# Optimization experiments

Measured on AMD Instinct MI355X. Metric: run time of the kernel, lower is better.

The kernel has to match this reference:

```python
import jax, jax.numpy as jnp
import numpy as np

B, S, E, H = 2, 2048, 1024, 16
HD = E // H  # head_dim = 64
NEG = jnp.float32(-1e9)


def setup_inputs() -> dict:
    key = jax.random.key(0)
    k1, k2, k3 = jax.random.split(key, 3)
    x = jax.random.normal(k1, (B, S, E), dtype=jnp.float32)
    w_qkv = jax.random.normal(k2, (E, 3 * E), dtype=jnp.float32) * 0.02
    b_qkv = jnp.zeros((3 * E,), dtype=jnp.float32)
    w_proj = jax.random.normal(k3, (E, E), dtype=jnp.float32) * 0.02
    b_proj = jnp.zeros((E,), dtype=jnp.float32)
    return {"x": x, "w_qkv": w_qkv, "b_qkv": b_qkv, "w_proj": w_proj, "b_proj": b_proj}


def reference(x, w_qkv, b_qkv, w_proj, b_proj):
    # c_attn (GPT2 Conv1D): x @ W + b -> [B,S,3E]
    qkv = x @ w_qkv + b_qkv
    q, k, v = jnp.split(qkv, 3, axis=-1)
    # split heads -> [B,H,S,HD]
    def heads(t):
        return t.reshape(B, S, H, HD).transpose(0, 2, 1, 3)
    q, k, v = heads(q), heads(k), heads(v)
    # scaled QK^T, causal mask, softmax (attn_pdrop=0 so dropout is identity)
    scores = jnp.einsum("bhqd,bhkd->bhqk", q, k) / jnp.sqrt(jnp.float32(HD))
    causal = jnp.tril(jnp.ones((S, S), dtype=bool))
    scores = jnp.where(causal, scores, NEG)
    attn = jax.nn.softmax(scores, axis=-1)
    out = jnp.einsum("bhqk,bhkd->bhqd", attn, v)
    out = out.transpose(0, 2, 1, 3).reshape(B, S, E)
    # c_proj
    return out @ w_proj + b_proj
```

## Files before the change

### kernel.cpp

```cpp
#include <hip/hip_runtime.h>


typedef __bf16 bf16;
typedef __bf16 bf16x4 __attribute__((ext_vector_type(4)));
typedef __bf16 bf16x8 __attribute__((ext_vector_type(8)));
typedef float f32x4 __attribute__((ext_vector_type(4)));

#define GLOBAL_AS(p) ((const __attribute__((address_space(1))) void*)(p))
#define LDS_AS(p) ((__attribute__((address_space(3))) void*)(p))

__device__ __forceinline__ void g2l16(const void* g, void* l) {
  __builtin_amdgcn_global_load_lds(GLOBAL_AS(g), LDS_AS(l), 16, 0, 0);
}

#define QSCL 0.18033688f

__global__ __launch_bounds__(256) void prep_kernel(
    const float* __restrict__ x, const float* __restrict__ wq,
    const float* __restrict__ wp, bf16* __restrict__ Xbf,
    bf16* __restrict__ Wqt, bf16* __restrict__ Wpt) {
  __shared__ float tile[32][33];
  const int t = threadIdx.x;
  const int b = blockIdx.x;
  if (b < 4096) {
    const int i = (b * 256 + t) * 4;
    const float4 v = *(const float4*)(x + i);
    bf16x4 o;
    o.x = (bf16)v.x; o.y = (bf16)v.y; o.z = (bf16)v.z; o.w = (bf16)v.w;
    *(bf16x4*)(Xbf + i) = o;
    return;
  }
  const float* W; bf16* Wt; int C, bx, by;
  if (b < 7168) {
    const int b2 = b - 4096;
    W = wq; Wt = Wqt; C = 3072; bx = b2 % 96; by = b2 / 96;
  } else {
    const int b3 = b - 7168;
    W = wp; Wt = Wpt; C = 1024; bx = b3 & 31; by = b3 >> 5;
  }
  const int c0 = bx * 32, r0 = by * 32;
  const int tx = t & 31, ty = t >> 5;
#pragma unroll
  for (int i = ty; i < 32; i += 8) tile[i][tx] = W[(r0 + i) * C + c0 + tx];
  __syncthreads();
#pragma unroll
  for (int i = ty; i < 32; i += 8)
    Wt[(c0 + i) * 1024 + r0 + tx] = (bf16)tile[tx][i];
}

template <int N, int EPI>
__global__ __launch_bounds__(256) void gemm_bt_kernel(
    const bf16* __restrict__ A, const bf16* __restrict__ Bt,
    const float* __restrict__ bias, float* __restrict__ Cf,
    bf16* __restrict__ Qo, bf16* __restrict__ Ko, bf16* __restrict__ Vo) {
  constexpr int K = 1024;
  __shared__ bf16 As[128 * 32];
  __shared__ bf16 Bs[128 * 32];
  const int t = threadIdx.x;
  const int m0 = blockIdx.x * 128;
  const int n0 = blockIdx.y * 128;
  const int wave = t >> 6, lane = t & 63;
  const int wr = (wave >> 1) * 64, wc = (wave & 1) * 64;
  const int lr = lane & 15, lg = lane >> 4;
  f32x4 acc[4][4] = {};
  const bf16* ag = A + (m0 + (t >> 2)) * K + (t & 3) * 8;
  const bf16* bg = Bt + (n0 + (t >> 2)) * K + (t & 3) * 8;
  for (int k0 = 0; k0 < K; k0 += 32) {
    __syncthreads();
    g2l16(ag, &As[t * 8]);
    g2l16(ag + 64 * K, &As[2048 + t * 8]);
    g2l16(bg, &Bs[t * 8]);
    g2l16(bg + 64 * K, &Bs[2048 + t * 8]);
    ag += 32; bg += 32;
    __syncthreads();
    bf16x8 af[4], bfr[4];
#pragma unroll
    for (int i = 0; i < 4; i++)
      af[i] = *(const bf16x8*)&As[(wr + i * 16 + lr) * 32 + lg * 8];
#pragma unroll
    for (int j = 0; j < 4; j++)
      bfr[j] = *(const bf16x8*)&Bs[(wc + j * 16 + lr) * 32 + lg * 8];
#pragma unroll
    for (int i = 0; i < 4; i++)
#pragma unroll
      for (int j = 0; j < 4; j++)
        acc[i][j] = __builtin_amdgcn_mfma_f32_16x16x32_bf16(af[i], bfr[j],
                                                            acc[i][j], 0, 0, 0);
  }
#pragma unroll
  for (int i = 0; i < 4; i++) {
#pragma unroll
    for (int j = 0; j < 4; j++) {
      const int n = n0 + wc + j * 16 + lr;
      const float bv = bias[n];
#pragma unroll
      for (int r = 0; r < 4; r++) {
        const int m = m0 + wr + i * 16 + lg * 4 + r;
        const float v = acc[i][j][r] + bv;
        if (EPI == 0) {
          Cf[m * N + n] = v;
        } else {
          const int b = m >> 11, s = m & 2047;
          const int reg = n >> 10, e = n & 1023;
          const int h = e >> 6, d = e & 63;
          bf16* dst = (reg == 0) ? Qo : (reg == 1) ? Ko : Vo;
          const float vv = (reg == 0) ? v * QSCL : v;
          dst[((b * 16 + h) * 2048 + s) * 64 + d] = (bf16)vv;
        }
      }
    }
  }
}

__global__ __launch_bounds__(256) void vtrans_kernel(
    const bf16* __restrict__ V, bf16* __restrict__ Vt) {
  __shared__ bf16 tile[64][72];
  const int t = threadIdx.x;
  const int bh = blockIdx.y;
  const int s0 = blockIdx.x * 64;
#pragma unroll
  for (int i = 0; i < 2; i++) {
    const int u = i * 256 + t;
    const int s = u >> 3, c = u & 7;
    *(bf16x8*)&tile[s][c * 8] =
        *(const bf16x8*)(V + ((size_t)bh * 2048 + s0 + s) * 64 + c * 8);
  }
  __syncthreads();
  {
    const int d = t >> 2, part = t & 3;
    bf16x8 o0, o1;
#pragma unroll
    for (int e = 0; e < 8; e++) {
      o0[e] = tile[part * 16 + e][d];
      o1[e] = tile[part * 16 + 8 + e][d];
    }
    bf16* dst = Vt + ((size_t)bh * 64 + d) * 2048 + s0 + part * 16;
    *(bf16x8*)dst = o0;
    *(bf16x8*)(dst + 8) = o1;
  }
}

__device__ __forceinline__ void stage_kv(const bf16* __restrict__ Kg,
                                         const bf16* __restrict__ Vg, int kb,
                                         bf16* ks, bf16* vs, int t) {
  int u = t, r = u >> 3, c = (u & 7) ^ (r & 7);
  g2l16(Kg + (kb + r) * 64 + c * 8, ks + u * 8);
  g2l16(Vg + r * 2048 + kb + c * 8, vs + u * 8);
  u = 256 + t; r = u >> 3; c = (u & 7) ^ (r & 7);
  g2l16(Kg + (kb + r) * 64 + c * 8, ks + u * 8);
  g2l16(Vg + r * 2048 + kb + c * 8, vs + u * 8);
}

__global__ __launch_bounds__(256, 3) void attn_kernel(
    const bf16* __restrict__ Qb, const bf16* __restrict__ Kb,
    const bf16* __restrict__ Vt, bf16* __restrict__ Obf) {
  __shared__ bf16 Ks[2][64 * 64];
  __shared__ bf16 Vs[2][64 * 64];
  __shared__ bf16 Ps[4][16 * 72];
  const int t = threadIdx.x;
  const int w = t >> 6, lane = t & 63;
  const int lr = lane & 15, lg = lane >> 4;
  const int bx = blockIdx.x;
  const int xcd = bx & 7, idx = bx >> 3;
  const int bh = (idx & 3) * 8 + xcd;
  const int strip = 31 - (idx >> 2);
  const int qb = strip * 64 + w * 16;
  const bf16* Qg = Qb + (size_t)bh * 2048 * 64;
  const bf16* Kg = Kb + (size_t)bh * 2048 * 64;
  const bf16* Vg = Vt + (size_t)bh * 64 * 2048;
  bf16x8 bq[2];
#pragma unroll
  for (int h = 0; h < 2; h++)
    bq[h] = *(const bf16x8*)(Qg + (qb + lr) * 64 + h * 32 + lg * 8);
  f32x4 oacc[4] = {};
  float lsum = 0.f;
  bf16* ps = &Ps[w][0];
  const int T = strip + 1;
  stage_kv(Kg, Vg, 0, Ks[0], Vs[0], t);
  for (int ti = 0; ti < T; ++ti) {
    __syncthreads();
    if (ti + 1 < T)
      stage_kv(Kg, Vg, (ti + 1) * 64, Ks[(ti + 1) & 1], Vs[(ti + 1) & 1], t);
    const int kb = ti * 64;
    const bf16* ks = Ks[ti & 1];
    const bf16* vs = Vs[ti & 1];
    bf16x8 ak[4][2], av[4][2];
#pragma unroll
    for (int j = 0; j < 4; j++) {
      const int row = j * 16 + lr;
#pragma unroll
      for (int h = 0; h < 2; h++)
        ak[j][h] =
            *(const bf16x8*)(ks + (row * 8 + ((h * 4 + lg) ^ (row & 7))) * 8);
    }
#pragma unroll
    for (int dt = 0; dt < 4; dt++) {
      const int row = dt * 16 + lr;
#pragma unroll
      for (int h = 0; h < 2; h++)
        av[dt][h] =
            *(const bf16x8*)(vs + (row * 8 + ((h * 4 + lg) ^ (row & 7))) * 8);
    }
    f32x4 sacc[4];
#pragma unroll
    for (int j = 0; j < 4; j++) {
      f32x4 s = {};
      s = __builtin_amdgcn_mfma_f32_16x16x32_bf16(ak[j][0], bq[0], s, 0, 0, 0);
      s = __builtin_amdgcn_mfma_f32_16x16x32_bf16(ak[j][1], bq[1], s, 0, 0, 0);
      sacc[j] = s;
    }
    const bool diag = (kb + 63 > qb);
    bf16x4 pk[4];
#pragma unroll
    for (int j = 0; j < 4; j++)
#pragma unroll
      for (int r = 0; r < 4; r++) {
        float v = sacc[j][r];
        if (diag && (kb + j * 16 + lg * 4 + r > qb + lr)) v = -1e30f;
        const float e = __builtin_amdgcn_exp2f(v);
        lsum += e;
        pk[j][r] = (bf16)e;
      }
    asm volatile("" ::: "memory");
#pragma unroll
    for (int j = 0; j < 4; j++)
      *(bf16x4*)(ps + lr * 72 + j * 16 + lg * 4) = pk[j];
    asm volatile("s_waitcnt lgkmcnt(0)" ::: "memory");
    bf16x8 bp[2];
#pragma unroll
    for (int h = 0; h < 2; h++)
      bp[h] = *(const bf16x8*)(ps + lr * 72 + h * 32 + lg * 8);
#pragma unroll
    for (int dt = 0; dt < 4; dt++) {
      f32x4 o = oacc[dt];
      o = __builtin_amdgcn_mfma_f32_16x16x32_bf16(av[dt][0], bp[0], o, 0, 0, 0);
      o = __builtin_amdgcn_mfma_f32_16x16x32_bf16(av[dt][1], bp[1], o, 0, 0, 0);
      oacc[dt] = o;
    }
  }
  lsum += __shfl_xor(lsum, 16, 64);
  lsum += __shfl_xor(lsum, 32, 64);
  const float inv = 1.0f / lsum;
  const int b = bh >> 4, hh = bh & 15;
  const int q = qb + lr;
  bf16* orow = Obf + ((size_t)(b * 2048 + q)) * 1024 + hh * 64;
#pragma unroll
  for (int dt = 0; dt < 4; dt++) {
    bf16x4 ov;
#pragma unroll
    for (int r = 0; r < 4; r++) ov[r] = (bf16)(oacc[dt][r] * inv);
    *(bf16x4*)(orow + dt * 16 + lg * 4) = ov;
  }
}

extern "C" void kernel_launch(void* const* d_in, const int* in_sizes, int n_in,
                              void* d_out, int out_size, void* d_ws,
                              size_t ws_size, hipStream_t stream) {
  const float* x      = (const float*)d_in[0];
  const float* w_qkv  = (const float*)d_in[1];
  const float* b_qkv  = (const float*)d_in[2];
  const float* w_proj = (const float*)d_in[3];
  const float* b_proj = (const float*)d_in[4];
  float* out = (float*)d_out;

  char* w = (char*)d_ws;
  bf16* Xbf = (bf16*)w;  w += 4096 * 1024 * 2;
  bf16* Wqt = (bf16*)w;  w += 3072 * 1024 * 2;
  bf16* Wpt = (bf16*)w;  w += 1024 * 1024 * 2;
  bf16* Qb  = (bf16*)w;  w += 2 * 16 * 2048 * 64 * 2;
  bf16* Kb  = (bf16*)w;  w += 2 * 16 * 2048 * 64 * 2;
  bf16* Vb  = (bf16*)w;  w += 2 * 16 * 2048 * 64 * 2;
  bf16* Obf = (bf16*)w;  w += 4096 * 1024 * 2;
  bf16* Vt  = Xbf;

  prep_kernel<<<8192, 256, 0, stream>>>(x, w_qkv, w_proj, Xbf, Wqt, Wpt);
  gemm_bt_kernel<3072, 1><<<dim3(32, 24), 256, 0, stream>>>(
      Xbf, Wqt, b_qkv, nullptr, Qb, Kb, Vb);
  vtrans_kernel<<<dim3(32, 32), 256, 0, stream>>>(Vb, Vt);
  attn_kernel<<<1024, 256, 0, stream>>>(Qb, Kb, Vt, Obf);
  gemm_bt_kernel<1024, 0><<<dim3(32, 8), 256, 0, stream>>>(
      Obf, Wpt, b_proj, out, nullptr, nullptr, nullptr);
}
```

Baseline: 181.5 us.

## Fuse V transpose into QKV GEMM, single-buffer attention, smaller proj tiles

The QKV GEMM epilogue now writes V directly in transposed [bh,d,s] layout with 4-wide stores, which removes the separate vtrans kernel and its extra round trip through memory. The attention kernel drops double-buffered K/V staging in favour of a single buffer with an extra barrier and raises its occupancy hint to 4 blocks per CU. This gives up load/compute overlap in exchange for more resident waves. The projection GEMM uses 64-row tiles so it launches twice as many blocks and fills more CUs.

```diff
diff --git a/kernel.cpp b/kernel.cpp
--- a/kernel.cpp
+++ b/kernel.cpp
@@ -48,11 +48,10 @@
     Wt[(c0 + i) * 1024 + r0 + tx] = (bf16)tile[tx][i];
 }
 
-template <int N, int EPI>
-__global__ __launch_bounds__(256) void gemm_bt_kernel(
+__global__ __launch_bounds__(256) void gemm_qkv_kernel(
     const bf16* __restrict__ A, const bf16* __restrict__ Bt,
-    const float* __restrict__ bias, float* __restrict__ Cf,
-    bf16* __restrict__ Qo, bf16* __restrict__ Ko, bf16* __restrict__ Vo) {
+    const float* __restrict__ bias, bf16* __restrict__ Qo,
+    bf16* __restrict__ Ko, bf16* __restrict__ Vto) {
   constexpr int K = 1024;
   __shared__ bf16 As[128 * 32];
   __shared__ bf16 Bs[128 * 32];
@@ -93,50 +92,78 @@
     for (int j = 0; j < 4; j++) {
       const int n = n0 + wc + j * 16 + lr;
       const float bv = bias[n];
+      if (n0 >= 2048) {
+        const int e = n & 1023, h = e >> 6, d = e & 63;
+        const int mb = m0 + wr + i * 16 + lg * 4;
+        const int b = mb >> 11, s = mb & 2047;
+        bf16x4 vv;
+#pragma unroll
+        for (int r = 0; r < 4; r++) vv[r] = (bf16)(acc[i][j][r] + bv);
+        *(bf16x4*)(Vto + ((size_t)((b * 16 + h) * 64 + d)) * 2048 + s) = vv;
+      } else {
+        const int e = n & 1023, h = e >> 6, d = e & 63;
+        const bool isq = (n < 1024);
+        bf16* dst = isq ? Qo : Ko;
+#pragma unroll
+        for (int r = 0; r < 4; r++) {
+          const int m = m0 + wr + i * 16 + lg * 4 + r;
+          const int b = m >> 11, s = m & 2047;
+          const float v = acc[i][j][r] + bv;
+          dst[((b * 16 + h) * 2048 + s) * 64 + d] = (bf16)(isq ? v * QSCL : v);
+        }
+      }
+    }
+  }
+}
+
+__global__ __launch_bounds__(256) void gemm_proj_kernel(
+    const bf16* __restrict__ A, const bf16* __restrict__ Bt,
+    const float* __restrict__ bias, float* __restrict__ Cf) {
+  constexpr int K = 1024, N = 1024;
+  __shared__ bf16 As[64 * 32];
+  __shared__ bf16 Bs[128 * 32];
+  const int t = threadIdx.x;
+  const int m0 = blockIdx.x * 64;
+  const int n0 = blockIdx.y * 128;
+  const int wave = t >> 6, lane = t & 63;
+  const int wr = (wave >> 1) * 32, wc = (wave & 1) * 64;
+  const int lr = lane & 15, lg = lane >> 4;
+  f32x4 acc[2][4] = {};
+  const bf16* ag = A + (m0 + (t >> 2)) * K + (t & 3) * 8;
+  const bf16* bg = Bt + (n0 + (t >> 2)) * K + (t & 3) * 8;
+  for (int k0 = 0; k0 < K; k0 += 32) {
+    __syncthreads();
+    g2l16(ag, &As[t * 8]);
+    g2l16(bg, &Bs[t * 8]);
+    g2l16(bg + 64 * K, &Bs[2048 + t * 8]);
+    ag += 32; bg += 32;
+    __syncthreads();
+    bf16x8 af[2], bfr[4];
+#pragma unroll
+    for (int i = 0; i < 2; i++)
+      af[i] = *(const bf16x8*)&As[(wr + i * 16 + lr) * 32 + lg * 8];
+#pragma unroll
+    for (int j = 0; j < 4; j++)
+      bfr[j] = *(const bf16x8*)&Bs[(wc + j * 16 + lr) * 32 + lg * 8];
+#pragma unroll
+    for (int i = 0; i < 2; i++)
+#pragma unroll
+      for (int j = 0; j < 4; j++)
+        acc[i][j] = __builtin_amdgcn_mfma_f32_16x16x32_bf16(af[i], bfr[j],
+                                                            acc[i][j], 0, 0, 0);
+  }
+#pragma unroll
+  for (int i = 0; i < 2; i++) {
+#pragma unroll
+    for (int j = 0; j < 4; j++) {
+      const int n = n0 + wc + j * 16 + lr;
+      const float bv = bias[n];
 #pragma unroll
       for (int r = 0; r < 4; r++) {
         const int m = m0 + wr + i * 16 + lg * 4 + r;
-        const float v = acc[i][j][r] + bv;
-        if (EPI == 0) {
-          Cf[m * N + n] = v;
-        } else {
-          const int b = m >> 11, s = m & 2047;
-          const int reg = n >> 10, e = n & 1023;
-          const int h = e >> 6, d = e & 63;
-          bf16* dst = (reg == 0) ? Qo : (reg == 1) ? Ko : Vo;
-          const float vv = (reg == 0) ? v * QSCL : v;
-          dst[((b * 16 + h) * 2048 + s) * 64 + d] = (bf16)vv;
-        }
+        Cf[m * N + n] = acc[i][j][r] + bv;
       }
     }
-  }
-}
-
-__global__ __launch_bounds__(256) void vtrans_kernel(
-    const bf16* __restrict__ V, bf16* __restrict__ Vt) {
-  __shared__ bf16 tile[64][72];
-  const int t = threadIdx.x;
-  const int bh = blockIdx.y;
-  const int s0 = blockIdx.x * 64;
-#pragma unroll
-  for (int i = 0; i < 2; i++) {
-    const int u = i * 256 + t;
-    const int s = u >> 3, c = u & 7;
-    *(bf16x8*)&tile[s][c * 8] =
-        *(const bf16x8*)(V + ((size_t)bh * 2048 + s0 + s) * 64 + c * 8);
-  }
-  __syncthreads();
-  {
-    const int d = t >> 2, part = t & 3;
-    bf16x8 o0, o1;
-#pragma unroll
-    for (int e = 0; e < 8; e++) {
-      o0[e] = tile[part * 16 + e][d];
-      o1[e] = tile[part * 16 + 8 + e][d];
-    }
-    bf16* dst = Vt + ((size_t)bh * 64 + d) * 2048 + s0 + part * 16;
-    *(bf16x8*)dst = o0;
-    *(bf16x8*)(dst + 8) = o1;
   }
 }
 
@@ -151,11 +178,11 @@
   g2l16(Vg + r * 2048 + kb + c * 8, vs + u * 8);
 }
 
-__global__ __launch_bounds__(256, 3) void attn_kernel(
+__global__ __launch_bounds__(256, 4) void attn_kernel(
     const bf16* __restrict__ Qb, const bf16* __restrict__ Kb,
     const bf16* __restrict__ Vt, bf16* __restrict__ Obf) {
-  __shared__ bf16 Ks[2][64 * 64];
-  __shared__ bf16 Vs[2][64 * 64];
+  __shared__ bf16 Ks[64 * 64];
+  __shared__ bf16 Vs[64 * 64];
   __shared__ bf16 Ps[4][16 * 72];
   const int t = threadIdx.x;
   const int w = t >> 6, lane = t & 63;
@@ -176,14 +203,11 @@
   float lsum = 0.f;
   bf16* ps = &Ps[w][0];
   const int T = strip + 1;
-  stage_kv(Kg, Vg, 0, Ks[0], Vs[0], t);
   for (int ti = 0; ti < T; ++ti) {
     __syncthreads();
-    if (ti + 1 < T)
-      stage_kv(Kg, Vg, (ti + 1) * 64, Ks[(ti + 1) & 1], Vs[(ti + 1) & 1], t);
+    stage_kv(Kg, Vg, ti * 64, Ks, Vs, t);
+    __syncthreads();
     const int kb = ti * 64;
-    const bf16* ks = Ks[ti & 1];
-    const bf16* vs = Vs[ti & 1];
     bf16x8 ak[4][2], av[4][2];
 #pragma unroll
     for (int j = 0; j < 4; j++) {
@@ -191,7 +215,7 @@
 #pragma unroll
       for (int h = 0; h < 2; h++)
         ak[j][h] =
-            *(const bf16x8*)(ks + (row * 8 + ((h * 4 + lg) ^ (row & 7))) * 8);
+            *(const bf16x8*)(Ks + (row * 8 + ((h * 4 + lg) ^ (row & 7))) * 8);
     }
 #pragma unroll
     for (int dt = 0; dt < 4; dt++) {
@@ -199,7 +223,7 @@
 #pragma unroll
       for (int h = 0; h < 2; h++)
         av[dt][h] =
-            *(const bf16x8*)(vs + (row * 8 + ((h * 4 + lg) ^ (row & 7))) * 8);
+            *(const bf16x8*)(Vs + (row * 8 + ((h * 4 + lg) ^ (row & 7))) * 8);
     }
     f32x4 sacc[4];
 #pragma unroll
@@ -269,15 +293,12 @@
   bf16* Wpt = (bf16*)w;  w += 1024 * 1024 * 2;
   bf16* Qb  = (bf16*)w;  w += 2 * 16 * 2048 * 64 * 2;
   bf16* Kb  = (bf16*)w;  w += 2 * 16 * 2048 * 64 * 2;
-  bf16* Vb  = (bf16*)w;  w += 2 * 16 * 2048 * 64 * 2;
+  bf16* Vt  = (bf16*)w;  w += 2 * 16 * 64 * 2048 * 2;
   bf16* Obf = (bf16*)w;  w += 4096 * 1024 * 2;
-  bf16* Vt  = Xbf;
 
   prep_kernel<<<8192, 256, 0, stream>>>(x, w_qkv, w_proj, Xbf, Wqt, Wpt);
-  gemm_bt_kernel<3072, 1><<<dim3(32, 24), 256, 0, stream>>>(
-      Xbf, Wqt, b_qkv, nullptr, Qb, Kb, Vb);
-  vtrans_kernel<<<dim3(32, 32), 256, 0, stream>>>(Vb, Vt);
+  gemm_qkv_kernel<<<dim3(32, 24), 256, 0, stream>>>(
+      Xbf, Wqt, b_qkv, Qb, Kb, Vt);
   attn_kernel<<<1024, 256, 0, stream>>>(Qb, Kb, Vt, Obf);
-  gemm_bt_kernel<1024, 0><<<dim3(32, 8), 256, 0, stream>>>(
-      Obf, Wpt, b_proj, out, nullptr, nullptr, nullptr);
-}
+  gemm_proj_kernel<<<dim3(64, 8), 256, 0, stream>>>(Obf, Wpt, b_proj, out);
+}
```

After: 170.1 us. -6.2%, faster.
